# Optimization experiments

Hardware: AMD Instinct MI355X
Metric: run time of the kernel (lower is better)

## Reference

```python
import jax, jax.numpy as jnp
import numpy as np
from jax import lax

IMG, P, C, D, H, L, B = 256, 16, 3, 768, 12, 8, 2
G = IMG // P            # 16
N = G * G               # 256 patches
FF = 2048               # hard-coded FFN hidden dim in ViTBlockWithCCAttention
DH = D // H
EPS = 1e-5


def setup_inputs() -> dict:
    key = jax.random.key(0)
    ks = jax.random.split(key, 24)
    s = 0.02
    rn = lambda k, shp: jax.random.normal(k, shp, jnp.float32) * s
    inp = {
        "x": jax.random.normal(ks[0], (B, C, IMG, IMG), jnp.float32),
        "patch_w": rn(ks[1], (D, C * P * P)),
        "patch_b": rn(ks[2], (D,)),
        "pos_embed": rn(ks[3], (1, N, D)),
        # per-layer stacked params (shared nn.MultiheadAttention per block)
        "in_proj_w": rn(ks[4], (L, 3 * D, D)),
        "in_proj_b": rn(ks[5], (L, 3 * D)),
        "out_w": rn(ks[6], (L, D, D)),
        "out_b": rn(ks[7], (L, D)),
        "ln1_g": jnp.ones((L, D), jnp.float32),
        "ln1_b": jnp.zeros((L, D), jnp.float32),
        "ln2_g": jnp.ones((L, D), jnp.float32),
        "ln2_b": jnp.zeros((L, D), jnp.float32),
        "ffn_w1": rn(ks[8], (L, FF, D)),
        "ffn_b1": rn(ks[9], (L, FF)),
        "ffn_w2": rn(ks[10], (L, D, FF)),
        "ffn_b2": rn(ks[11], (L, D)),
        "edge_w": rn(ks[12], (D, 1)),
        "edge_b": rn(ks[13], (D,)),
        "conv1_w": rn(ks[14], (256, D, 3, 3)),
        "conv1_b": rn(ks[15], (256,)),
        "conv2_w": rn(ks[16], (1, 256, 1, 1)),
        "conv2_b": rn(ks[17], (1,)),
    }
    return inp


def _ln(z, g, b):
    m = z.mean(-1, keepdims=True)
    v = ((z - m) ** 2).mean(-1, keepdims=True)
    return (z - m) / jnp.sqrt(v + EPS) * g + b


def _mha(z, wi, bi, wo, bo):
    # z: (M, S, D). Returns out (M,S,D) and head-averaged attn weights (M,S,S)
    M, S, _ = z.shape
    qkv = z @ wi.T + bi
    q, k, v = jnp.split(qkv, 3, axis=-1)
    sp = lambda t: t.reshape(M, S, H, DH).transpose(0, 2, 1, 3)  # (M,H,S,dh)
    q, k, v = sp(q), sp(k), sp(v)
    a = jax.nn.softmax(jnp.einsum('mhqd,mhkd->mhqk', q, k) / np.sqrt(DH).astype(np.float32), axis=-1)
    o = jnp.einsum('mhqk,mhkd->mhqd', a, v).transpose(0, 2, 1, 3).reshape(M, S, D)
    return o @ wo.T + bo, a.mean(1)


def reference(x, patch_w, patch_b, pos_embed, in_proj_w, in_proj_b, out_w, out_b,
              ln1_g, ln1_b, ln2_g, ln2_b, ffn_w1, ffn_b1, ffn_w2, ffn_b2,
              edge_w, edge_b, conv1_w, conv1_b, conv2_w, conv2_b):
    Bc = x.shape[0]
    # patch embedding: unfold -> (B, N, C*P*P) -> linear
    patches = x.reshape(Bc, C, G, P, G, P).transpose(0, 2, 4, 1, 3, 5).reshape(Bc, N, C * P * P)
    h = patches @ patch_w.T + patch_b + pos_embed

    edge_sum = jnp.zeros((Bc, N, D), h.dtype)
    for i in range(L):
        xl = _ln(h, ln1_g[i], ln1_b[i])
        x2d = xl.reshape(Bc, G, G, D)
        # rows: sequences along height, one per column
        row_x = x2d.transpose(0, 2, 1, 3).reshape(Bc * G, G, D)
        row_out, row_a = _mha(row_x, in_proj_w[i], in_proj_b[i], out_w[i], out_b[i])
        # cols: sequences along width, one per row
        col_x = x2d.reshape(Bc * G, G, D)
        col_out, col_a = _mha(col_x, in_proj_w[i], in_proj_b[i], out_w[i], out_b[i])
        attn_out = (row_out.reshape(Bc, G, G, D).transpose(0, 2, 1, 3)
                    + col_out.reshape(Bc, G, G, D)).reshape(Bc, N, D)
        h = h + attn_out
        z = _ln(h, ln2_g[i], ln2_b[i])
        h = h + jax.nn.relu(z @ ffn_w1[i].T + ffn_b1[i]) @ ffn_w2[i].T + ffn_b2[i]
        # attention-divergence edge tokens (query-averaged attn maps)
        div = jnp.abs(row_a.mean(1) - col_a.mean(1)).reshape(Bc, N, 1)
        edge_sum = edge_sum + (div @ edge_w.T + edge_b)
    h = h + edge_sum / L

    feat = h.transpose(0, 2, 1).reshape(Bc, D, G, G)
    feat = jax.image.resize(feat, (Bc, D, IMG, IMG), method="bilinear")  # align_corners=False
    dn = ("NCHW", "OIHW", "NCHW")
    y = lax.conv_general_dilated(feat, conv1_w, (1, 1), "SAME", dimension_numbers=dn)
    y = jax.nn.relu(y + conv1_b[None, :, None, None])
    y = lax.conv_general_dilated(y, conv2_w, (1, 1), "SAME", dimension_numbers=dn)
    return y + conv2_b[None, :, None, None]
```

## Files before the change

### kernel.cpp

```cpp
#include <hip/hip_runtime.h>
#include <hip/hip_bf16.h>
#include <math.h>

#define BB 2
#define CIN 3
#define IMGS 256
#define PS 16
#define GG 16
#define NN 256
#define DIM 768
#define NH 12
#define NL 8
#define FFD 2048
#define LNEPS 1e-5f

typedef __attribute__((ext_vector_type(8))) short bf16x8;
typedef __attribute__((ext_vector_type(8))) unsigned short u16x8;
typedef __attribute__((ext_vector_type(4))) float f32x4;

#define MB     1
#define MB2    2
#define MPOS   4
#define MRELU  8
#define MRES   16
#define MOBF16 32
#define MAS2   64
#define MLNA   256
#define MAIM2  512

#define LW_IPW  0
#define LW_OUTW 1769472
#define LW_FW1  2359296
#define LW_FW2  3932160
#define LW_TOT  5505024
#define WCT_N   1769472
#define PW_N    589824

__device__ inline unsigned short bc(float f) {
    return __builtin_bit_cast(unsigned short, __float2bfloat16(f));
}
__device__ inline float fbc(unsigned short u) {
    unsigned int x = ((unsigned int)u) << 16;
    return __builtin_bit_cast(float, x);
}

__device__ inline void gload16(const unsigned short* g, unsigned short* l) {
    __builtin_amdgcn_global_load_lds((const __attribute__((address_space(1))) void*)g,
                                     (__attribute__((address_space(3))) void*)l, 16, 0, 0);
}

template<int MODE, int BN>
__global__ __launch_bounds__(256) void gemm_bf16(
    const void* __restrict__ Av, const void* __restrict__ A2v,
    const unsigned short* __restrict__ B16,
    const float* __restrict__ bias, const float* __restrict__ pos,
    const float2* __restrict__ stats,
    const float* __restrict__ lng, const float* __restrict__ lnb,
    float* __restrict__ C, unsigned short* __restrict__ C16,
    int M, int N, int K, int zdiv,
    long long sAo, long long sBi, long long sCo, long long sCi)
{
    constexpr int NI = BN / 32;
    int z = blockIdx.y;
    int zo = z / zdiv, zi = z % zdiv;
    const unsigned short* A16 = (const unsigned short*)Av + (size_t)zo * sAo;
    const float* Af  = (const float*)Av  + (size_t)zo * sAo;
    const float* Af2 = (const float*)A2v + (size_t)zo * sAo;
    B16 += (size_t)zi * sBi;
    long long coff = (long long)zo * sCo + (long long)zi * sCi;

    int NBY = M >> 5;
    int nbysh = 31 - __builtin_clz(NBY);
    int id = blockIdx.x;
    int qch = gridDim.x >> 3;
    int wgid = (id & 7) * qch + (id >> 3);
    int bx = wgid >> nbysh, by = wgid & (NBY - 1);
    int bm = by * 32, bn = bx * BN;

    __shared__ __align__(16) unsigned short As[2][2048], Bs[2][BN * 64];
    int tid = threadIdx.x;
    int lane = tid & 63, wave = tid >> 6;
    int wr = wave >> 1, wc = wave & 1;
    int sA = tid;
    int srowA = sA >> 3, schkA = (sA & 7) ^ (srowA & 7);

    f32x4 acc[NI] = {};
    f32x4 rA0, rA1, rA20, rA21, gv0, gv1, bv0, bv1;
    float2 strow;

    auto gstageA = [&](int b, int kt) {
        gload16(A16 + (size_t)(bm + srowA) * K + kt * 64 + schkA * 8, &As[b][sA * 8]);
    };
    auto gstageB = [&](int b, int kt) {
        #pragma unroll
        for (int i = 0; i < NI; ++i) {
            int s = tid + i * 256;
            int row = s >> 3, chk = (s & 7) ^ (row & 7);
            gload16(B16 + (size_t)(bn + row) * K + kt * 64 + chk * 8, &Bs[b][s * 8]);
        }
    };
    auto ldA = [&](int kt) {
        int k0 = kt * 64 + schkA * 8;
        if constexpr (MODE & MAIM2) {
            int m = bm + srowA;
            int bq = m >> 8, n = m & 255, gy = n >> 4, gx = n & 15;
            int c = k0 >> 8, rem = k0 & 255, py = rem >> 4, px = rem & 15;
            const float* src = Af + (((size_t)(bq * CIN + c) * IMGS + gy * PS + py) << 8)
                             + gx * PS + px;
            rA0 = *(const f32x4*)(src);
            rA1 = *(const f32x4*)(src + 4);
        } else {
            size_t off = (size_t)(bm + srowA) * K + k0;
            rA0 = *(const f32x4*)(Af + off);
            rA1 = *(const f32x4*)(Af + off + 4);
            if constexpr (MODE & MAS2) {
                rA20 = *(const f32x4*)(Af2 + off);
                rA21 = *(const f32x4*)(Af2 + off + 4);
            }
            if constexpr (MODE & MLNA) {
                strow = stats[bm + srowA];
                gv0 = *(const f32x4*)(lng + k0); gv1 = *(const f32x4*)(lng + k0 + 4);
                bv0 = *(const f32x4*)(lnb + k0); bv1 = *(const f32x4*)(lnb + k0 + 4);
            }
        }
    };
    auto wrA = [&](int b) {
        bf16x8 v;
        #pragma unroll
        for (int j = 0; j < 4; ++j) {
            float x0 = rA0[j], x1 = rA1[j];
            if constexpr (MODE & MAS2) { x0 += rA20[j]; x1 += rA21[j]; }
            if constexpr (MODE & MLNA) {
                x0 = (x0 - strow.x) * strow.y * gv0[j] + bv0[j];
                x1 = (x1 - strow.x) * strow.y * gv1[j] + bv1[j];
            }
            v[j] = (short)bc(x0); v[4 + j] = (short)bc(x1);
        }
        *(bf16x8*)(&As[b][sA * 8]) = v;
    };
    constexpr bool regA = (MODE & (MAS2 | MLNA | MAIM2)) != 0;
    auto compute = [&](int b) {
        const unsigned short* Ab = As[b];
        const unsigned short* Bb = Bs[b];
        int rl = lane & 15, kh = lane >> 4;
        #pragma unroll
        for (int ks = 0; ks < 2; ++ks) {
            int kc = ks * 4 + kh;
            int ar = 16 * wr + rl;
            bf16x8 af = *(const bf16x8*)(Ab + ar * 64 + (kc ^ (ar & 7)) * 8);
            #pragma unroll
            for (int ni = 0; ni < NI; ++ni) {
                int br = 16 * NI * wc + 16 * ni + rl;
                bf16x8 bf = *(const bf16x8*)(Bb + br * 64 + (kc ^ (br & 7)) * 8);
                acc[ni] = __builtin_amdgcn_mfma_f32_16x16x32_bf16(af, bf, acc[ni], 0, 0, 0);
            }
        }
    };

    int nt = K >> 6;
    if constexpr (!regA) gstageA(0, 0); else { ldA(0); wrA(0); }
    gstageB(0, 0);
    __syncthreads();
    int buf = 0;
    for (int t = 0; t < nt; ++t) {
        if (t + 1 < nt) {
            if constexpr (!regA) gstageA(buf ^ 1, t + 1); else ldA(t + 1);
            gstageB(buf ^ 1, t + 1);
        }
        compute(buf);
        if (t + 1 < nt) {
            if constexpr (regA) wrA(buf ^ 1);
        }
        __syncthreads();
        buf ^= 1;
    }

    #pragma unroll
    for (int ni = 0; ni < NI; ++ni) {
        #pragma unroll
        for (int r = 0; r < 4; ++r) {
            int row = bm + 16 * wr + (lane >> 4) * 4 + r;
            int col = bn + 16 * NI * wc + 16 * ni + (lane & 15);
            float v = acc[ni][r];
            if (MODE & (MB | MB2)) v += bias[col] * ((MODE & MB2) ? 2.f : 1.f);
            if (MODE & MPOS) v += pos[(size_t)(row & (NN - 1)) * N + col];
            if (MODE & MRELU) v = fmaxf(v, 0.f);
            long long ci = coff + (long long)row * N + col;
            if (MODE & MOBF16) C16[ci] = bc(v);
            else if (MODE & MRES) C[ci] += v;
            else C[ci] = v;
        }
    }
}

__global__ __launch_bounds__(256) void cvtmega_kernel(
    const float* __restrict__ conv1_w, const float* __restrict__ patch_w,
    const float* __restrict__ ipw, const float* __restrict__ ow,
    const float* __restrict__ f1, const float* __restrict__ f2,
    unsigned short* __restrict__ dst)
{
    long long i = (long long)(blockIdx.x * 256 + threadIdx.x) * 8;
    u16x8 v;
    if (i < WCT_N) {
        int c = (int)(i % DIM);
        int t = (int)(i / DIM);
        int oc = t & 255, dydx = t >> 8;
        const float* src = conv1_w + ((size_t)oc * DIM + c) * 9 + dydx;
        #pragma unroll
        for (int j = 0; j < 8; ++j) v[j] = bc(src[j * 9]);
    } else if (i < WCT_N + PW_N) {
        const float* src = patch_w + (i - WCT_N);
        f32x4 a = *(const f32x4*)(src), b = *(const f32x4*)(src + 4);
        #pragma unroll
        for (int j = 0; j < 4; ++j) { v[j] = bc(a[j]); v[4 + j] = bc(b[j]); }
    } else {
        long long r0 = i - (WCT_N + PW_N);
        int l = (int)(r0 / LW_TOT);
        int r = (int)(r0 - (long long)l * LW_TOT);
        const float* src; long long off;
        if (r < LW_OUTW)      { src = ipw; off = (long long)l * 1769472 + r; }
        else if (r < LW_FW1)  { src = ow;  off = (long long)l * 589824 + (r - LW_OUTW); }
        else if (r < LW_FW2)  { src = f1;  off = (long long)l * 1572864 + (r - LW_FW1); }
        else                  { src = f2;  off = (long long)l * 1572864 + (r - LW_FW2); }
        f32x4 a = *(const f32x4*)(src + off), b = *(const f32x4*)(src + off + 4);
        #pragma unroll
        for (int j = 0; j < 4; ++j) { v[j] = bc(a[j]); v[4 + j] = bc(b[j]); }
    }
    *(u16x8*)(dst + i) = v;
}

__global__ void cvtlayer_kernel(const float* __restrict__ ipw, const float* __restrict__ ow,
                                const float* __restrict__ f1, const float* __restrict__ f2,
                                unsigned short* __restrict__ dst)
{
    int i = (blockIdx.x * 256 + threadIdx.x) * 8;
    const float* src; int off;
    if (i < LW_OUTW)      { src = ipw; off = i; }
    else if (i < LW_FW1)  { src = ow;  off = i - LW_OUTW; }
    else if (i < LW_FW2)  { src = f1;  off = i - LW_FW1; }
    else                  { src = f2;  off = i - LW_FW2; }
    f32x4 a = *(const f32x4*)(src + off), b = *(const f32x4*)(src + off + 4);
    u16x8 v;
    #pragma unroll
    for (int j = 0; j < 4; ++j) { v[j] = bc(a[j]); v[4 + j] = bc(b[j]); }
    *(u16x8*)(dst + i) = v;
}

__global__ __launch_bounds__(256) void lnstat_kernel(const float* __restrict__ X,
                                                     float2* __restrict__ st)
{
    int row = blockIdx.x * 4 + (threadIdx.x >> 6);
    int lane = threadIdx.x & 63;
    const float* xp = X + (size_t)row * DIM + lane * 4;
    float s = 0.f, s2 = 0.f;
    #pragma unroll
    for (int seg = 0; seg < 3; ++seg) {
        f32x4 v = *(const f32x4*)(xp + seg * 256);
        s += v[0] + v[1] + v[2] + v[3];
        s2 += v[0] * v[0] + v[1] * v[1] + v[2] * v[2] + v[3] * v[3];
    }
    #pragma unroll
    for (int off = 32; off > 0; off >>= 1) {
        s  += __shfl_xor(s, off);
        s2 += __shfl_xor(s2, off);
    }
    if (lane == 0) {
        float mean = s * (1.f / DIM);
        float var = s2 * (1.f / DIM) - mean * mean;
        st[row] = make_float2(mean, rsqrtf(var + LNEPS));
    }
}

__global__ __launch_bounds__(256) void attn_kernel(
    const float* __restrict__ qkv, float* __restrict__ orow,
    float* __restrict__ ocol, float* __restrict__ amh)
{
    int b = blockIdx.x >> 4, g = blockIdx.x & 15;
    int type = blockIdx.y;
    int hh = blockIdx.z;
    int tid = threadIdx.x;
    __shared__ float qs[16][68], ks[16][68], vs[16][68], as_[16][17];
    {
        int sr = tid >> 4, dq = tid & 15;
        int n = (type == 0) ? (sr * GG + g) : (g * GG + sr);
        const float* base = qkv + (size_t)(b * NN + n) * (3 * DIM) + hh * 64 + dq * 4;
        float4 qv = *(const float4*)(base);
        float4 kv = *(const float4*)(base + DIM);
        float4 vv = *(const float4*)(base + 2 * DIM);
        *(float4*)&qs[sr][dq * 4] = qv;
        *(float4*)&ks[sr][dq * 4] = kv;
        *(float4*)&vs[sr][dq * 4] = vv;
    }
    __syncthreads();
    int s = tid >> 4, t = tid & 15;
    float sc = 0.f;
    #pragma unroll
    for (int d = 0; d < 64; ++d) sc += qs[s][d] * ks[t][d];
    sc *= 0.125f;
    float mx = sc;
    #pragma unroll
    for (int off = 1; off < 16; off <<= 1) mx = fmaxf(mx, __shfl_xor(mx, off, 16));
    float p = __expf(sc - mx);
    float sum = p;
    #pragma unroll
    for (int off = 1; off < 16; off <<= 1) sum += __shfl_xor(sum, off, 16);
    as_[s][t] = p / sum;
    __syncthreads();
    if (tid < 16) {
        float a = 0.f;
        #pragma unroll
        for (int ss = 0; ss < 16; ++ss) a += as_[ss][tid];
        amh[((size_t)(type * BB + b) * NN + g * GG + tid) * NH + hh] = a;
    }
    int s2 = tid >> 4, dg = (tid & 15) * 4;
    float o0 = 0, o1 = 0, o2 = 0, o3 = 0;
    #pragma unroll
    for (int t2 = 0; t2 < 16; ++t2) {
        float a2 = as_[s2][t2];
        o0 += a2 * vs[t2][dg];
        o1 += a2 * vs[t2][dg + 1];
        o2 += a2 * vs[t2][dg + 2];
        o3 += a2 * vs[t2][dg + 3];
    }
    int n2 = (type == 0) ? (s2 * GG + g) : (g * GG + s2);
    float* op = ((type == 0) ? orow : ocol) + (size_t)(b * NN + n2) * DIM + hh * 64 + dg;
    *(float4*)op = make_float4(o0, o1, o2, o3);
}

__global__ __launch_bounds__(256) void hfin_kernel(
    const float* __restrict__ h, const float* __restrict__ amh,
    const float* __restrict__ ew, const float* __restrict__ eb,
    unsigned short* __restrict__ hf)
{
    int m = blockIdx.x;
    int b = m >> 8, n = m & 255;
    int tid = threadIdx.x;
    __shared__ float divs;
    if (tid < 8) {
        const float* base = amh + (size_t)tid * 12288 + (size_t)b * 3072 + n * 12;
        float rs = 0.f, cs = 0.f;
        #pragma unroll
        for (int hh = 0; hh < NH; ++hh) {
            rs += base[hh];
            cs += base[6144 + hh];
        }
        float d = fabsf(rs - cs);
        d += __shfl_xor(d, 1);
        d += __shfl_xor(d, 2);
        d += __shfl_xor(d, 4);
        if (tid == 0) divs = d * (1.f / (NH * GG)) * (1.f / NL);
    }
    __syncthreads();
    float dv = divs;
    const float* hp = h + (size_t)m * DIM;
    unsigned short* yp = hf + (size_t)m * DIM;
    #pragma unroll
    for (int seg = 0; seg < 3; ++seg) {
        int d0 = tid + seg * 256;
        yp[d0] = bc(hp[d0] + dv * ew[d0] + eb[d0]);
    }
}

__global__ __launch_bounds__(256) void s_kernel(const float* __restrict__ P,
                                               unsigned short* __restrict__ S16)
{
    int bdy = blockIdx.y;
    int b = bdy / 3, dy = bdy % 3;
    int ocg = blockIdx.x;
    __shared__ float Pl[3][4][16][17];
    int tid = threadIdx.x;
    #pragma unroll
    for (int l = 0; l < 12; ++l) {
        int e = l * 256 + tid;
        int dx = e >> 10, rem = e & 1023;
        int oc = rem >> 8, pix = rem & 255;
        int i = pix >> 4, j = pix & 15;
        Pl[dx][oc][j][i] =
            P[(((size_t)b * 9 + dy * 3 + dx) * 256 + ocg * 4 + oc) * 256 + pix];
    }
    __syncthreads();
    int xq = tid >> 6, oc = (tid >> 4) & 3, i = tid & 15;
    for (int xx = 0; xx < 64; ++xx) {
        int x = xq * 64 + xx;
        float acc = 0.f;
        #pragma unroll
        for (int dx = 0; dx < 3; ++dx) {
            int u = x + dx - 1;
            float p = (u + 0.5f) * 0.0625f - 0.5f;
            float fl = floorf(p);
            float f = p - fl;
            int j0 = (int)fl;
            int ja = j0 < 0 ? 0 : j0;
            int jb = (j0 + 1 > 15) ? 15 : (j0 + 1);
            bool valid = (u >= 0) && (u <= 255);
            float w0 = valid ? 1.f - f : 0.f;
            float w1 = valid ? f : 0.f;
            acc += w0 * Pl[dx][oc][ja][i] + w1 * Pl[dx][oc][jb][i];
        }
        S16[(((size_t)(b * 256 + x) * 3 + dy) * 256 + ocg * 4 + oc) * 16 + i] = bc(acc);
    }
}

__global__ __launch_bounds__(256) void out_kernel(
    const unsigned short* __restrict__ S16, const float* __restrict__ b1,
    const float* __restrict__ w2, const float* __restrict__ b2p,
    float* __restrict__ out)
{
    int b = blockIdx.x >> 8, x = blockIdx.x & 255;
    __shared__ float Sl[12288];
    const unsigned short* Sp = S16 + (size_t)(b * 256 + x) * 12288;
    #pragma unroll
    for (int c = 0; c < 6; ++c) {
        int l8 = (c * 256 + threadIdx.x) * 8;
        u16x8 v = *(const u16x8*)(Sp + l8);
        #pragma unroll
        for (int j = 0; j < 8; ++j) Sl[l8 + j] = fbc(v[j]);
    }
    __syncthreads();
    int y = threadIdx.x;
    float wy[3][2];
    int iy[3][2];
    #pragma unroll
    for (int dy = 0; dy < 3; ++dy) {
        int v = y + dy - 1;
        if (v < 0 || v > 255) {
            wy[dy][0] = wy[dy][1] = 0.f;
            iy[dy][0] = iy[dy][1] = 0;
        } else {
            float pp = (v + 0.5f) * 0.0625f - 0.5f;
            float fl = floorf(pp);
            float f = pp - fl;
            int i0 = (int)fl;
            iy[dy][0] = i0 < 0 ? 0 : i0;
            iy[dy][1] = (i0 + 1 > 15) ? 15 : (i0 + 1);
            wy[dy][0] = 1.f - f;
            wy[dy][1] = f;
        }
    }
    float acc = 0.f;
    for (int oc = 0; oc < 256; ++oc) {
        float sv = 0.f;
        #pragma unroll
        for (int dy = 0; dy < 3; ++dy)
            sv += wy[dy][0] * Sl[dy * 4096 + oc * 16 + iy[dy][0]]
                + wy[dy][1] * Sl[dy * 4096 + oc * 16 + iy[dy][1]];
        sv += b1[oc];
        acc += fmaxf(sv, 0.f) * w2[oc];
    }
    out[(size_t)b * 65536 + y * 256 + x] = acc + b2p[0];
}

extern "C" void kernel_launch(void* const* d_in, const int* in_sizes, int n_in,
                              void* d_out, int out_size, void* d_ws, size_t ws_size,
                              hipStream_t stream)
{
    const float* x         = (const float*)d_in[0];
    const float* patch_w   = (const float*)d_in[1];
    const float* patch_b   = (const float*)d_in[2];
    const float* pos_embed = (const float*)d_in[3];
    const float* in_proj_w = (const float*)d_in[4];
    const float* in_proj_b = (const float*)d_in[5];
    const float* out_w     = (const float*)d_in[6];
    const float* out_b     = (const float*)d_in[7];
    const float* ln1_g     = (const float*)d_in[8];
    const float* ln1_b     = (const float*)d_in[9];
    const float* ln2_g     = (const float*)d_in[10];
    const float* ln2_b     = (const float*)d_in[11];
    const float* ffn_w1    = (const float*)d_in[12];
    const float* ffn_b1    = (const float*)d_in[13];
    const float* ffn_w2    = (const float*)d_in[14];
    const float* ffn_b2    = (const float*)d_in[15];
    const float* edge_w    = (const float*)d_in[16];
    const float* edge_b    = (const float*)d_in[17];
    const float* conv1_w   = (const float*)d_in[18];
    const float* conv1_b   = (const float*)d_in[19];
    const float* conv2_w   = (const float*)d_in[20];
    const float* conv2_b   = (const float*)d_in[21];
    float* out = (float*)d_out;
    float* ws = (float*)d_ws;

    float* h      = ws;
    float* qkv    = h + 393216;
    float* orow   = qkv + 1179648;
    float* ocol   = orow + 393216;
    float* Pb     = ocol + 393216;
    float* amh    = Pb + 1179648;
    float2* stats = (float2*)(amh + 98304);
    unsigned short* Sb16   = (unsigned short*)(stats + 512);
    unsigned short* hid16  = Sb16 + 6291456;
    unsigned short* hfin16 = hid16 + 1048576;
    unsigned short* Wct16  = hfin16 + 393216;
    unsigned short* pw16   = Wct16 + 1769472;
    unsigned short* lw16   = pw16 + 589824;

    size_t base_shorts = 6291456 + 1048576 + 393216 + 1769472 + 589824;
    size_t base_bytes = (size_t)(393216 + 1179648 + 393216 + 393216 + 1179648 + 98304 + 1024) * 4
                      + base_shorts * 2;
    bool big = ws_size >= base_bytes + (size_t)8 * LW_TOT * 2;

    {
        long long nel = WCT_N + PW_N + (big ? 8LL * LW_TOT : 0LL);
        int nblk = (int)(nel / (8 * 256));
        cvtmega_kernel<<<dim3(nblk), 256, 0, stream>>>(
            conv1_w, patch_w, in_proj_w, out_w, ffn_w1, ffn_w2, Wct16);
    }

    gemm_bf16<MB | MPOS | MAIM2, 32><<<dim3(24 * 16), 256, 0, stream>>>(
        x, nullptr, pw16, patch_b, pos_embed, nullptr, nullptr, nullptr,
        h, nullptr, 512, 768, 768, 1, 0, 0, 0, 0);

    for (int l = 0; l < NL; ++l) {
        const unsigned short* lw = big ? lw16 + (size_t)l * LW_TOT : lw16;
        if (!big)
            cvtlayer_kernel<<<dim3(2688), 256, 0, stream>>>(
                in_proj_w + (size_t)l * 1769472, out_w + (size_t)l * 589824,
                ffn_w1 + (size_t)l * 1572864, ffn_w2 + (size_t)l * 1572864, lw16);
        lnstat_kernel<<<dim3(128), 256, 0, stream>>>(h, stats);
        gemm_bf16<MB | MLNA, 64><<<dim3(36 * 16), 256, 0, stream>>>(
            h, nullptr, lw + LW_IPW, in_proj_b + (size_t)l * 2304, nullptr,
            stats, ln1_g + l * DIM, ln1_b + l * DIM, qkv, nullptr,
            512, 2304, 768, 1, 0, 0, 0, 0);
        attn_kernel<<<dim3(BB * GG, 2, NH), 256, 0, stream>>>(
            qkv, orow, ocol, amh + (size_t)l * 12288);
        gemm_bf16<MB2 | MRES | MAS2, 32><<<dim3(24 * 16), 256, 0, stream>>>(
            orow, ocol, lw + LW_OUTW, out_b + (size_t)l * DIM, nullptr,
            nullptr, nullptr, nullptr, h, nullptr,
            512, 768, 768, 1, 0, 0, 0, 0);
        lnstat_kernel<<<dim3(128), 256, 0, stream>>>(h, stats);
        gemm_bf16<MB | MRELU | MOBF16 | MLNA, 64><<<dim3(32 * 16), 256, 0, stream>>>(
            h, nullptr, lw + LW_FW1, ffn_b1 + (size_t)l * FFD, nullptr,
            stats, ln2_g + l * DIM, ln2_b + l * DIM, nullptr, hid16,
            512, 2048, 768, 1, 0, 0, 0, 0);
        gemm_bf16<MB | MRES, 32><<<dim3(24 * 16), 256, 0, stream>>>(
            hid16, nullptr, lw + LW_FW2, ffn_b2 + (size_t)l * DIM, nullptr,
            nullptr, nullptr, nullptr, h, nullptr,
            512, 768, 2048, 1, 0, 0, 0, 0);
    }

    hfin_kernel<<<dim3(512), 256, 0, stream>>>(h, amh, edge_w, edge_b, hfin16);
    gemm_bf16<0, 32><<<dim3(8 * 8, 18), 256, 0, stream>>>(
        Wct16, nullptr, hfin16, nullptr, nullptr, nullptr, nullptr, nullptr,
        Pb, nullptr, 256, 256, 768,
        2, 196608LL, 196608LL, 65536LL, 589824LL);
    s_kernel<<<dim3(64, 6), 256, 0, stream>>>(Pb, Sb16);
    out_kernel<<<dim3(512), 256, 0, stream>>>(Sb16, conv1_b, conv2_w, conv2_b, out);
}
```

Baseline: 635.5 us.

## Fuse LayerNorm statistics into GEMM epilogues and restructure weight conversion

Removes the separate lnstat kernels by having the residual-writing GEMMs emit per-row partial sum and sum-of-squares (one slot per 16-column wave slice). The LN-consuming GEMMs then reduce these 48 partials per row into mean and rstd in shared memory at block start. The weight conversion kernel is also split into a 2D-grid segmented kernel, with the conv1 weight transpose now staged through shared memory for coalesced reads. This saves 16 kernel launches and the extra passes over h. The cost is shuffle reductions in the GEMM epilogue and stats computed as E[x^2]-mean^2 from partials, which is slightly less numerically robust.

New measurement: 605.2 us. -4.8%, faster.

```diff
diff --git a/kernel.cpp b/kernel.cpp
--- a/kernel.cpp
+++ b/kernel.cpp
@@ -27,6 +27,7 @@
 #define MAS2   64
 #define MLNA   256
 #define MAIM2  512
+#define MSTATP 1024
 
 #define LW_IPW  0
 #define LW_OUTW 1769472
@@ -54,8 +55,9 @@
     const void* __restrict__ Av, const void* __restrict__ A2v,
     const unsigned short* __restrict__ B16,
     const float* __restrict__ bias, const float* __restrict__ pos,
-    const float2* __restrict__ stats,
+    const float2* __restrict__ pstat,
     const float* __restrict__ lng, const float* __restrict__ lnb,
+    float2* __restrict__ pstatOut,
     float* __restrict__ C, unsigned short* __restrict__ C16,
     int M, int N, int K, int zdiv,
     long long sAo, long long sBi, long long sCo, long long sCi)
@@ -78,11 +80,31 @@
     int bm = by * 32, bn = bx * BN;
 
     __shared__ __align__(16) unsigned short As[2][2048], Bs[2][BN * 64];
+    __shared__ float2 sstat[32];
     int tid = threadIdx.x;
     int lane = tid & 63, wave = tid >> 6;
     int wr = wave >> 1, wc = wave & 1;
     int sA = tid;
     int srowA = sA >> 3, schkA = (sA & 7) ^ (srowA & 7);
+
+    if constexpr (MODE & MLNA) {
+        int row = tid >> 3, j = tid & 7;
+        const float2* pr = pstat + (size_t)(bm + row) * 48 + j * 6;
+        float s = 0.f, s2 = 0.f;
+        #pragma unroll
+        for (int k = 0; k < 6; ++k) { float2 v = pr[k]; s += v.x; s2 += v.y; }
+        #pragma unroll
+        for (int m2 = 1; m2 < 8; m2 <<= 1) {
+            s  += __shfl_xor(s, m2);
+            s2 += __shfl_xor(s2, m2);
+        }
+        if (j == 0) {
+            float mean = s * (1.f / DIM);
+            float var = s2 * (1.f / DIM) - mean * mean;
+            sstat[row] = make_float2(mean, rsqrtf(var + LNEPS));
+        }
+        __syncthreads();
+    }
 
     f32x4 acc[NI] = {};
     f32x4 rA0, rA1, rA20, rA21, gv0, gv1, bv0, bv1;
@@ -118,7 +140,7 @@
                 rA21 = *(const f32x4*)(Af2 + off + 4);
             }
             if constexpr (MODE & MLNA) {
-                strow = stats[bm + srowA];
+                strow = sstat[srowA];
                 gv0 = *(const f32x4*)(lng + k0); gv1 = *(const f32x4*)(lng + k0 + 4);
                 bv0 = *(const f32x4*)(lnb + k0); bv1 = *(const f32x4*)(lnb + k0 + 4);
             }
@@ -175,6 +197,7 @@
         buf ^= 1;
     }
 
+    float vfin[4];
     #pragma unroll
     for (int ni = 0; ni < NI; ++ni) {
         #pragma unroll
@@ -186,47 +209,76 @@
             if (MODE & MPOS) v += pos[(size_t)(row & (NN - 1)) * N + col];
             if (MODE & MRELU) v = fmaxf(v, 0.f);
             long long ci = coff + (long long)row * N + col;
-            if (MODE & MOBF16) C16[ci] = bc(v);
-            else if (MODE & MRES) C[ci] += v;
-            else C[ci] = v;
-        }
-    }
-}
-
-__global__ __launch_bounds__(256) void cvtmega_kernel(
+            if (MODE & MOBF16) { C16[ci] = bc(v); }
+            else if (MODE & MRES) { v += C[ci]; C[ci] = v; }
+            else { C[ci] = v; }
+            if (ni == 0) vfin[r] = v;
+        }
+    }
+    if constexpr (MODE & MSTATP) {
+        #pragma unroll
+        for (int r = 0; r < 4; ++r) {
+            float s = vfin[r], s2 = vfin[r] * vfin[r];
+            #pragma unroll
+            for (int m2 = 1; m2 < 16; m2 <<= 1) {
+                s  += __shfl_xor(s, m2);
+                s2 += __shfl_xor(s2, m2);
+            }
+            if ((lane & 15) == 0) {
+                int row = bm + 16 * wr + (lane >> 4) * 4 + r;
+                pstatOut[(size_t)row * 48 + bx * 2 + wc] = make_float2(s, s2);
+            }
+        }
+    }
+}
+
+__global__ __launch_bounds__(256) void cvtseg_kernel(
     const float* __restrict__ conv1_w, const float* __restrict__ patch_w,
     const float* __restrict__ ipw, const float* __restrict__ ow,
     const float* __restrict__ f1, const float* __restrict__ f2,
-    unsigned short* __restrict__ dst)
-{
-    long long i = (long long)(blockIdx.x * 256 + threadIdx.x) * 8;
-    u16x8 v;
-    if (i < WCT_N) {
-        int c = (int)(i % DIM);
-        int t = (int)(i / DIM);
-        int oc = t & 255, dydx = t >> 8;
-        const float* src = conv1_w + ((size_t)oc * DIM + c) * 9 + dydx;
-        #pragma unroll
-        for (int j = 0; j < 8; ++j) v[j] = bc(src[j * 9]);
-    } else if (i < WCT_N + PW_N) {
-        const float* src = patch_w + (i - WCT_N);
-        f32x4 a = *(const f32x4*)(src), b = *(const f32x4*)(src + 4);
+    unsigned short* __restrict__ Wct16, unsigned short* __restrict__ pw16,
+    unsigned short* __restrict__ lw16)
+{
+    int y = blockIdx.y;
+    int tid = threadIdx.x;
+    if (y == 0) {
+        int oc = blockIdx.x;
+        if (oc >= 256) return;
+        __shared__ float w[6912];
+        const float* src = conv1_w + (size_t)oc * 6912;
+        #pragma unroll
+        for (int k = 0; k < 27; ++k) w[tid + k * 256] = src[tid + k * 256];
+        __syncthreads();
+        #pragma unroll
+        for (int dydx = 0; dydx < 9; ++dydx) {
+            #pragma unroll
+            for (int k = 0; k < 3; ++k) {
+                int c = tid + k * 256;
+                Wct16[(size_t)dydx * 196608 + oc * 768 + c] = bc(w[c * 9 + dydx]);
+            }
+        }
+    } else if (y == 1) {
+        int i = (blockIdx.x * 256 + tid) * 8;
+        if (i >= PW_N) return;
+        f32x4 a = *(const f32x4*)(patch_w + i), b = *(const f32x4*)(patch_w + i + 4);
+        u16x8 v;
         #pragma unroll
         for (int j = 0; j < 4; ++j) { v[j] = bc(a[j]); v[4 + j] = bc(b[j]); }
+        *(u16x8*)(pw16 + i) = v;
     } else {
-        long long r0 = i - (WCT_N + PW_N);
-        int l = (int)(r0 / LW_TOT);
-        int r = (int)(r0 - (long long)l * LW_TOT);
-        const float* src; long long off;
-        if (r < LW_OUTW)      { src = ipw; off = (long long)l * 1769472 + r; }
-        else if (r < LW_FW1)  { src = ow;  off = (long long)l * 589824 + (r - LW_OUTW); }
-        else if (r < LW_FW2)  { src = f1;  off = (long long)l * 1572864 + (r - LW_FW1); }
-        else                  { src = f2;  off = (long long)l * 1572864 + (r - LW_FW2); }
+        int l = y - 2;
+        int r = (blockIdx.x * 256 + tid) * 8;
+        const float* src; int off;
+        if (r < LW_OUTW)      { src = ipw + (size_t)l * 1769472; off = r; }
+        else if (r < LW_FW1)  { src = ow  + (size_t)l * 589824;  off = r - LW_OUTW; }
+        else if (r < LW_FW2)  { src = f1  + (size_t)l * 1572864; off = r - LW_FW1; }
+        else                  { src = f2  + (size_t)l * 1572864; off = r - LW_FW2; }
         f32x4 a = *(const f32x4*)(src + off), b = *(const f32x4*)(src + off + 4);
+        u16x8 v;
         #pragma unroll
         for (int j = 0; j < 4; ++j) { v[j] = bc(a[j]); v[4 + j] = bc(b[j]); }
-    }
-    *(u16x8*)(dst + i) = v;
+        *(u16x8*)(lw16 + (size_t)l * LW_TOT + r) = v;
+    }
 }
 
 __global__ void cvtlayer_kernel(const float* __restrict__ ipw, const float* __restrict__ ow,
@@ -244,31 +296,6 @@
     #pragma unroll
     for (int j = 0; j < 4; ++j) { v[j] = bc(a[j]); v[4 + j] = bc(b[j]); }
     *(u16x8*)(dst + i) = v;
-}
-
-__global__ __launch_bounds__(256) void lnstat_kernel(const float* __restrict__ X,
-                                                     float2* __restrict__ st)
-{
-    int row = blockIdx.x * 4 + (threadIdx.x >> 6);
-    int lane = threadIdx.x & 63;
-    const float* xp = X + (size_t)row * DIM + lane * 4;
-    float s = 0.f, s2 = 0.f;
-    #pragma unroll
-    for (int seg = 0; seg < 3; ++seg) {
-        f32x4 v = *(const f32x4*)(xp + seg * 256);
-        s += v[0] + v[1] + v[2] + v[3];
-        s2 += v[0] * v[0] + v[1] * v[1] + v[2] * v[2] + v[3] * v[3];
-    }
-    #pragma unroll
-    for (int off = 32; off > 0; off >>= 1) {
-        s  += __shfl_xor(s, off);
-        s2 += __shfl_xor(s2, off);
-    }
-    if (lane == 0) {
-        float mean = s * (1.f / DIM);
-        float var = s2 * (1.f / DIM) - mean * mean;
-        st[row] = make_float2(mean, rsqrtf(var + LNEPS));
-    }
 }
 
 __global__ __launch_bounds__(256) void attn_kernel(
@@ -485,8 +512,8 @@
     float* ocol   = orow + 393216;
     float* Pb     = ocol + 393216;
     float* amh    = Pb + 1179648;
-    float2* stats = (float2*)(amh + 98304);
-    unsigned short* Sb16   = (unsigned short*)(stats + 512);
+    float2* pstat = (float2*)(amh + 98304);
+    unsigned short* Sb16   = (unsigned short*)(amh + 98304 + 49152);
     unsigned short* hid16  = Sb16 + 6291456;
     unsigned short* hfin16 = hid16 + 1048576;
     unsigned short* Wct16  = hfin16 + 393216;
@@ -494,19 +521,15 @@
     unsigned short* lw16   = pw16 + 589824;
 
     size_t base_shorts = 6291456 + 1048576 + 393216 + 1769472 + 589824;
-    size_t base_bytes = (size_t)(393216 + 1179648 + 393216 + 393216 + 1179648 + 98304 + 1024) * 4
+    size_t base_bytes = (size_t)(393216 + 1179648 + 393216 + 393216 + 1179648 + 98304 + 49152) * 4
                       + base_shorts * 2;
     bool big = ws_size >= base_bytes + (size_t)8 * LW_TOT * 2;
 
-    {
-        long long nel = WCT_N + PW_N + (big ? 8LL * LW_TOT : 0LL);
-        int nblk = (int)(nel / (8 * 256));
-        cvtmega_kernel<<<dim3(nblk), 256, 0, stream>>>(
-            conv1_w, patch_w, in_proj_w, out_w, ffn_w1, ffn_w2, Wct16);
-    }
-
-    gemm_bf16<MB | MPOS | MAIM2, 32><<<dim3(24 * 16), 256, 0, stream>>>(
-        x, nullptr, pw16, patch_b, pos_embed, nullptr, nullptr, nullptr,
+    cvtseg_kernel<<<dim3(2688, big ? 10 : 2), 256, 0, stream>>>(
+        conv1_w, patch_w, in_proj_w, out_w, ffn_w1, ffn_w2, Wct16, pw16, lw16);
+
+    gemm_bf16<MB | MPOS | MAIM2 | MSTATP, 32><<<dim3(24 * 16), 256, 0, stream>>>(
+        x, nullptr, pw16, patch_b, pos_embed, nullptr, nullptr, nullptr, pstat,
         h, nullptr, 512, 768, 768, 1, 0, 0, 0, 0);
 
     for (int l = 0; l < NL; ++l) {
@@ -515,31 +538,29 @@
             cvtlayer_kernel<<<dim3(2688), 256, 0, stream>>>(
                 in_proj_w + (size_t)l * 1769472, out_w + (size_t)l * 589824,
                 ffn_w1 + (size_t)l * 1572864, ffn_w2 + (size_t)l * 1572864, lw16);
-        lnstat_kernel<<<dim3(128), 256, 0, stream>>>(h, stats);
         gemm_bf16<MB | MLNA, 64><<<dim3(36 * 16), 256, 0, stream>>>(
             h, nullptr, lw + LW_IPW, in_proj_b + (size_t)l * 2304, nullptr,
-            stats, ln1_g + l * DIM, ln1_b + l * DIM, qkv, nullptr,
+            pstat, ln1_g + l * DIM, ln1_b + l * DIM, nullptr, qkv, nullptr,
             512, 2304, 768, 1, 0, 0, 0, 0);
         attn_kernel<<<dim3(BB * GG, 2, NH), 256, 0, stream>>>(
             qkv, orow, ocol, amh + (size_t)l * 12288);
-        gemm_bf16<MB2 | MRES | MAS2, 32><<<dim3(24 * 16), 256, 0, stream>>>(
+        gemm_bf16<MB2 | MRES | MAS2 | MSTATP, 32><<<dim3(24 * 16), 256, 0, stream>>>(
             orow, ocol, lw + LW_OUTW, out_b + (size_t)l * DIM, nullptr,
-            nullptr, nullptr, nullptr, h, nullptr,
+            nullptr, nullptr, nullptr, pstat, h, nullptr,
             512, 768, 768, 1, 0, 0, 0, 0);
-        lnstat_kernel<<<dim3(128), 256, 0, stream>>>(h, stats);
         gemm_bf16<MB | MRELU | MOBF16 | MLNA, 64><<<dim3(32 * 16), 256, 0, stream>>>(
             h, nullptr, lw + LW_FW1, ffn_b1 + (size_t)l * FFD, nullptr,
-            stats, ln2_g + l * DIM, ln2_b + l * DIM, nullptr, hid16,
+            pstat, ln2_g + l * DIM, ln2_b + l * DIM, nullptr, nullptr, hid16,
             512, 2048, 768, 1, 0, 0, 0, 0);
-        gemm_bf16<MB | MRES, 32><<<dim3(24 * 16), 256, 0, stream>>>(
+        gemm_bf16<MB | MRES | MSTATP, 32><<<dim3(24 * 16), 256, 0, stream>>>(
             hid16, nullptr, lw + LW_FW2, ffn_b2 + (size_t)l * DIM, nullptr,
-            nullptr, nullptr, nullptr, h, nullptr,
+            nullptr, nullptr, nullptr, pstat, h, nullptr,
             512, 768, 2048, 1, 0, 0, 0, 0);
     }
 
     hfin_kernel<<<dim3(512), 256, 0, stream>>>(h, amh, edge_w, edge_b, hfin16);
     gemm_bf16<0, 32><<<dim3(8 * 8, 18), 256, 0, stream>>>(
-        Wct16, nullptr, hfin16, nullptr, nullptr, nullptr, nullptr, nullptr,
+        Wct16, nullptr, hfin16, nullptr, nullptr, nullptr, nullptr, nullptr, nullptr,
         Pb, nullptr, 256, 256, 768,
         2, 196608LL, 196608LL, 65536LL, 589824LL);
     s_kernel<<<dim3(64, 6), 256, 0, stream>>>(Pb, Sb16);
```
